# Kernel optimization log

Measured on AMD Instinct MI355X. Metric: run time of the kernel, lower is better.

Reference implementation:

```python
import jax, jax.numpy as jnp
import numpy as np

NH, NKV, HD = 32, 8, 64
ROPE_BASE = 10000.0


def _rope_tables(L, hd):
    inv_freq = 1.0 / (ROPE_BASE ** (jnp.arange(0, hd, 2, dtype=jnp.float32) / hd))
    t = jnp.arange(L, dtype=jnp.float32)
    freqs = jnp.outer(t, inv_freq)              # (L, hd/2)
    emb = jnp.concatenate([freqs, freqs], -1)   # (L, hd)
    return jnp.cos(emb), jnp.sin(emb)


def _rotate_half(x):
    h = x.shape[-1] // 2
    return jnp.concatenate([-x[..., h:], x[..., :h]], axis=-1)


def _apply_rope(x, cos, sin):
    # x: (B, H, L, hd); cos/sin: (L, hd) broadcast over B, H
    return x * cos[None, None] + _rotate_half(x) * sin[None, None]


def setup_inputs() -> dict:
    key = jax.random.key(0)
    ks = jax.random.split(key, 5)
    B, L, H = 2, 2048, 2048
    s = 0.02
    return {
        "x": jax.random.normal(ks[0], (B, L, H), dtype=jnp.float32),
        "wq": jax.random.normal(ks[1], (NH * HD, H), dtype=jnp.float32) * s,
        "wk": jax.random.normal(ks[2], (NKV * HD, H), dtype=jnp.float32) * s,
        "wv": jax.random.normal(ks[3], (NKV * HD, H), dtype=jnp.float32) * s,
        "wo": jax.random.normal(ks[4], (H, NH * HD), dtype=jnp.float32) * s,
    }


def reference(x, wq, wk, wv, wo):
    B, L, H = x.shape
    rep = NH // NKV
    q = (x @ wq.T).reshape(B, L, NH, HD).transpose(0, 2, 1, 3)    # (B, nh, L, hd)
    k = (x @ wk.T).reshape(B, L, NKV, HD).transpose(0, 2, 1, 3)   # (B, nkv, L, hd)
    v = (x @ wv.T).reshape(B, L, NKV, HD).transpose(0, 2, 1, 3)
    cos, sin = _rope_tables(L, HD)
    q = _apply_rope(q, cos, sin)
    k = _apply_rope(k, cos, sin)
    # GQA: group q heads instead of repeating K/V (same math as repeat_interleave)
    qg = q.reshape(B, NKV, rep, L, HD)
    scores = jnp.einsum("bgrqd,bgkd->bgrqk", qg, k) / jnp.sqrt(jnp.float32(HD))
    causal = jnp.tril(jnp.ones((L, L), dtype=bool))
    scores = jnp.where(causal, scores, jnp.float32(-jnp.inf))
    probs = jax.nn.softmax(scores, axis=-1)
    out = jnp.einsum("bgrqk,bgkd->bgrqd", probs, v)               # (B, nkv, rep, L, hd)
    out = out.reshape(B, NH, L, HD).transpose(0, 2, 1, 3).reshape(B, L, NH * HD)
    return out @ wo.T
```

## Files before the change

kernel.cpp:

```cpp
#include <hip/hip_runtime.h>

using u16 = unsigned short;
using u32 = unsigned int;
typedef __attribute__((ext_vector_type(8))) short bf16x8;
typedef __attribute__((ext_vector_type(4))) float f32x4;
typedef __attribute__((ext_vector_type(4))) float float4v;
typedef __attribute__((ext_vector_type(4))) unsigned short us4;
typedef __attribute__((ext_vector_type(2))) unsigned int u32x2;

__device__ __forceinline__ u16 f2bf(float f) {
  union { float f; unsigned u; } v; v.f = f;
  unsigned r = v.u + 0x7fffu + ((v.u >> 16) & 1u);
  return (u16)(r >> 16);
}

__device__ __forceinline__ u32 cvtpk(float a, float b) {
  u32 r;
  asm("v_cvt_pk_bf16_f32 %0, %1, %2" : "=v"(r) : "v"(a), "v"(b));
  return r;
}

__device__ __forceinline__ void glds16(const void* g, void* l) {
  __builtin_amdgcn_global_load_lds(
      (const __attribute__((address_space(1))) void*)g,
      (__attribute__((address_space(3))) void*)l, 16, 0, 0);
}

__device__ __forceinline__ void lgkm0() {
  asm volatile("s_waitcnt lgkmcnt(0)" ::: "memory");
}

#define TILE_GATE()                                      \
  asm volatile("s_waitcnt vmcnt(0)" ::: "memory");       \
  __builtin_amdgcn_s_barrier();                          \
  __builtin_amdgcn_sched_barrier(0);

#define MFMA(a, b, c) __builtin_amdgcn_mfma_f32_16x16x32_bf16((a), (b), (c), 0, 0, 0)

#define QSCALE 0.1803368801111601f

__global__ __launch_bounds__(256) void cvt_all(
    const float* __restrict__ x, const float* __restrict__ wq,
    const float* __restrict__ wk, const float* __restrict__ wv,
    const float* __restrict__ wo, u16* __restrict__ x_bf,
    u16* __restrict__ wqkv, u16* __restrict__ wo_bf) {
  int i = blockIdx.x * 256 + threadIdx.x;
  const float4v* src;
  us4* dst;
  if (i < 2097152) {
    src = (const float4v*)x + i; dst = (us4*)x_bf + i;
  } else if (i < 3145728) {
    int j = i - 2097152; src = (const float4v*)wq + j; dst = (us4*)wqkv + j;
  } else if (i < 3407872) {
    int j = i - 3145728; src = (const float4v*)wk + j; dst = (us4*)wqkv + 1048576 + j;
  } else if (i < 3670016) {
    int j = i - 3407872; src = (const float4v*)wv + j; dst = (us4*)wqkv + 1310720 + j;
  } else {
    int j = i - 3670016; src = (const float4v*)wo + j; dst = (us4*)wo_bf + j;
  }
  float4v v = *src;
  us4 o;
  o[0] = f2bf(v[0]); o[1] = f2bf(v[1]); o[2] = f2bf(v[2]); o[3] = f2bf(v[3]);
  *dst = o;
}

__global__ __launch_bounds__(256) void rope_cs(float2* __restrict__ cs) {
  int i = blockIdx.x * 256 + threadIdx.x;
  if (i >= 2048 * 32) return;
  int t = i >> 5, fi = i & 31;
  float inv = powf(10000.f, -(float)fi / 32.f);
  float ang = (float)t * inv;
  cs[i] = make_float2(cosf(ang), sinf(ang));
}

__global__ __launch_bounds__(512, 2) void gemm_qkv(const u16* __restrict__ Ag,
                                                   const u16* __restrict__ Bg,
                                                   const float2* __restrict__ cs,
                                                   u16* __restrict__ q_r,
                                                   u16* __restrict__ k_r,
                                                   u16* __restrict__ v_t) {
  __shared__ u16 Al[2][256 * 64];
  __shared__ u16 Bl[2][256 * 64];

  const int nwg = gridDim.x;
  const int cpx = nwg >> 3;
  const int flat = blockIdx.x;
  const int swb = (flat & 7) * cpx + (flat >> 3);
  const int bx = swb & 15, by = swb >> 4;
  const int bmRow = bx * 256, bnRow = by * 256;

  const int tid = threadIdx.x;
  const int w = tid >> 6, l = tid & 63;
  const int wm = w >> 2, wn = w & 3;
  const int lr = l & 15, lg = l >> 4;
  const int rb7 = lr & 7;

  const int srow = l >> 3;
  const int sch = (l & 7) ^ srow;
  const int reg0 = w * 32;
  const u16* a_src = Ag + (size_t)(bmRow + reg0 + srow) * 2048 + sch * 8;
  const u16* b_src = Bg + (size_t)(bnRow + reg0 + srow) * 2048 + sch * 8;

  auto stageTile = [&](int kt, int bufi) {
    const int kc = kt * 64;
#pragma unroll
    for (int i = 0; i < 4; ++i)
      glds16(a_src + (size_t)i * 8 * 2048 + kc, &Al[bufi][(reg0 + i * 8) * 64]);
#pragma unroll
    for (int i = 0; i < 4; ++i)
      glds16(b_src + (size_t)i * 8 * 2048 + kc, &Bl[bufi][(reg0 + i * 8) * 64]);
  };
  auto rd = [&](const u16* base, int row, int g) -> bf16x8 {
    return *(const bf16x8*)((const char*)base + row * 128 + (((g) ^ rb7) << 4));
  };

  f32x4 acc[8][4];
#pragma unroll
  for (int m = 0; m < 8; ++m)
#pragma unroll
    for (int n = 0; n < 4; ++n) acc[m][n] = f32x4{0.f, 0.f, 0.f, 0.f};

  bf16x8 af[4][2], bfr[4][2];
  const int NT = 32;

  stageTile(0, 0);
  for (int t = 0; t < NT; ++t) {
    const int cur = t & 1;
    const u16* Ab = &Al[cur][0];
    const u16* Bb = &Bl[cur][0];

    TILE_GATE()
    if (t + 1 < NT) stageTile(t + 1, cur ^ 1);

#pragma unroll
    for (int m = 0; m < 4; ++m)
#pragma unroll
      for (int kk = 0; kk < 2; ++kk)
        af[m][kk] = rd(Ab, wm * 128 + m * 16 + lr, kk * 4 + lg);
#pragma unroll
    for (int n = 0; n < 2; ++n)
#pragma unroll
      for (int kk = 0; kk < 2; ++kk)
        bfr[n][kk] = rd(Bb, wn * 64 + n * 16 + lr, kk * 4 + lg);
    __builtin_amdgcn_s_barrier();
    __builtin_amdgcn_s_setprio(1);
#pragma unroll
    for (int m = 0; m < 4; ++m)
#pragma unroll
      for (int n = 0; n < 2; ++n)
#pragma unroll
        for (int kk = 0; kk < 2; ++kk)
          acc[m][n] = MFMA(af[m][kk], bfr[n][kk], acc[m][n]);
    __builtin_amdgcn_s_setprio(0);
    __builtin_amdgcn_s_barrier();

#pragma unroll
    for (int n = 2; n < 4; ++n)
#pragma unroll
      for (int kk = 0; kk < 2; ++kk)
        bfr[n][kk] = rd(Bb, wn * 64 + n * 16 + lr, kk * 4 + lg);
    __builtin_amdgcn_s_barrier();
    __builtin_amdgcn_s_setprio(1);
#pragma unroll
    for (int m = 0; m < 4; ++m)
#pragma unroll
      for (int n = 2; n < 4; ++n)
#pragma unroll
        for (int kk = 0; kk < 2; ++kk)
          acc[m][n] = MFMA(af[m][kk], bfr[n][kk], acc[m][n]);
    __builtin_amdgcn_s_setprio(0);
    __builtin_amdgcn_s_barrier();

#pragma unroll
    for (int m = 0; m < 4; ++m)
#pragma unroll
      for (int kk = 0; kk < 2; ++kk)
        af[m][kk] = rd(Ab, wm * 128 + 64 + m * 16 + lr, kk * 4 + lg);
    __builtin_amdgcn_s_barrier();
    __builtin_amdgcn_s_setprio(1);
#pragma unroll
    for (int m = 0; m < 4; ++m)
#pragma unroll
      for (int n = 0; n < 2; ++n)
#pragma unroll
        for (int kk = 0; kk < 2; ++kk)
          acc[4 + m][n] = MFMA(af[m][kk], bfr[n][kk], acc[4 + m][n]);
    __builtin_amdgcn_s_setprio(0);
    __builtin_amdgcn_s_barrier();

    __builtin_amdgcn_s_setprio(1);
#pragma unroll
    for (int m = 0; m < 4; ++m)
#pragma unroll
      for (int n = 2; n < 4; ++n)
#pragma unroll
        for (int kk = 0; kk < 2; ++kk)
          acc[4 + m][n] = MFMA(af[m][kk], bfr[n][kk], acc[4 + m][n]);
    __builtin_amdgcn_s_setprio(0);
  }

  const int cbcol = bnRow + wn * 64;
  const int rowbase = bmRow + wm * 128;

  if (cbcol < 2560) {
    const bool isQ = (cbcol < 2048);
    const int h = (isQ ? cbcol : cbcol - 2048) >> 6;
    u16* dst = isQ ? q_r : k_r;
    const int nh = isQ ? 32 : 8;
#pragma unroll
    for (int m = 0; m < 8; ++m) {
#pragma unroll
      for (int j = 0; j < 4; ++j) {
        const int row = rowbase + m * 16 + lg * 4 + j;
        const int b = row >> 11, ll = row & 2047;
        const float2 c0 = cs[ll * 32 + lr];
        const float2 c1 = cs[ll * 32 + 16 + lr];
        u16* op = dst + (((size_t)b * nh + h) * 2048 + ll) * 64;
#pragma unroll
        for (int n = 0; n < 4; ++n) {
          const float val = acc[m][n][j];
          const float oth = acc[m][n ^ 2][j];
          const float cx = (n & 1) ? c1.x : c0.x;
          const float sy = (n & 1) ? c1.y : c0.y;
          float r = (n < 2) ? (val * cx - oth * sy) : (val * cx + oth * sy);
          if (isQ) r *= QSCALE;
          op[n * 16 + lr] = f2bf(r);
        }
      }
    }
  } else {
    const int h = (cbcol - 2560) >> 6;
#pragma unroll
    for (int m = 0; m < 8; ++m) {
      const int row0 = rowbase + m * 16 + lg * 4;
      const int b = row0 >> 11, l0 = row0 & 2047;
#pragma unroll
      for (int n = 0; n < 4; ++n) {
        const int d = n * 16 + lr;
        us4 pk;
#pragma unroll
        for (int j = 0; j < 4; ++j) pk[j] = f2bf(acc[m][n][j]);
        *(us4*)&v_t[(((size_t)b * 8 + h) * 64 + d) * 2048 + l0] = pk;
      }
    }
  }
}

__global__ __launch_bounds__(512, 2) void gemm_o(const u16* __restrict__ Ag,
                                                 const u16* __restrict__ Bg,
                                                 float* __restrict__ C) {
  __shared__ u16 Al[2][256 * 64];
  __shared__ u16 Bl[2][128 * 64];

  const int nwg = gridDim.x;
  const int cpx = nwg >> 3;
  const int flat = blockIdx.x;
  const int swb = (flat & 7) * cpx + (flat >> 3);
  const int bx = swb & 15, by = swb >> 4;
  const int bmRow = bx * 256, bnRow = by * 128;

  const int tid = threadIdx.x;
  const int w = tid >> 6, l = tid & 63;
  const int wm = w >> 1, wn = w & 1;
  const int lr = l & 15, lg = l >> 4;
  const int rb7 = lr & 7;

  const int srow = l >> 3;
  const int sch = (l & 7) ^ srow;
  const int areg = w * 32;
  const int breg = w * 16;
  const u16* a_src = Ag + (size_t)(bmRow + areg + srow) * 2048 + sch * 8;
  const u16* b_src = Bg + (size_t)(bnRow + breg + srow) * 2048 + sch * 8;

  auto stageTile = [&](int kt, int bufi) {
    const int kc = kt * 64;
#pragma unroll
    for (int i = 0; i < 4; ++i)
      glds16(a_src + (size_t)i * 8 * 2048 + kc, &Al[bufi][(areg + i * 8) * 64]);
#pragma unroll
    for (int i = 0; i < 2; ++i)
      glds16(b_src + (size_t)i * 8 * 2048 + kc, &Bl[bufi][(breg + i * 8) * 64]);
  };
  auto rd = [&](const u16* base, int row, int g) -> bf16x8 {
    return *(const bf16x8*)((const char*)base + row * 128 + (((g) ^ rb7) << 4));
  };

  f32x4 acc[4][4];
#pragma unroll
  for (int m = 0; m < 4; ++m)
#pragma unroll
    for (int n = 0; n < 4; ++n) acc[m][n] = f32x4{0.f, 0.f, 0.f, 0.f};

  bf16x8 af[4][2], bfr[4][2];
  const int NT = 32;

  stageTile(0, 0);
  for (int t = 0; t < NT; ++t) {
    const int cur = t & 1;
    const u16* Ab = &Al[cur][0];
    const u16* Bb = &Bl[cur][0];

    TILE_GATE()
    if (t + 1 < NT) stageTile(t + 1, cur ^ 1);

#pragma unroll
    for (int m = 0; m < 4; ++m)
#pragma unroll
      for (int kk = 0; kk < 2; ++kk)
        af[m][kk] = rd(Ab, wm * 64 + m * 16 + lr, kk * 4 + lg);
#pragma unroll
    for (int n = 0; n < 2; ++n)
#pragma unroll
      for (int kk = 0; kk < 2; ++kk)
        bfr[n][kk] = rd(Bb, wn * 64 + n * 16 + lr, kk * 4 + lg);
    __builtin_amdgcn_s_barrier();
    __builtin_amdgcn_s_setprio(1);
#pragma unroll
    for (int m = 0; m < 4; ++m)
#pragma unroll
      for (int n = 0; n < 2; ++n)
#pragma unroll
        for (int kk = 0; kk < 2; ++kk)
          acc[m][n] = MFMA(af[m][kk], bfr[n][kk], acc[m][n]);
    __builtin_amdgcn_s_setprio(0);
    __builtin_amdgcn_s_barrier();

#pragma unroll
    for (int n = 2; n < 4; ++n)
#pragma unroll
      for (int kk = 0; kk < 2; ++kk)
        bfr[n][kk] = rd(Bb, wn * 64 + n * 16 + lr, kk * 4 + lg);
    __builtin_amdgcn_s_barrier();
    __builtin_amdgcn_s_setprio(1);
#pragma unroll
    for (int m = 0; m < 4; ++m)
#pragma unroll
      for (int n = 2; n < 4; ++n)
#pragma unroll
        for (int kk = 0; kk < 2; ++kk)
          acc[m][n] = MFMA(af[m][kk], bfr[n][kk], acc[m][n]);
    __builtin_amdgcn_s_setprio(0);
  }

  float* Cp = C + (size_t)(bmRow + wm * 64) * 2048 + bnRow + wn * 64;
#pragma unroll
  for (int m = 0; m < 4; ++m)
#pragma unroll
    for (int n = 0; n < 4; ++n)
#pragma unroll
      for (int j = 0; j < 4; ++j)
        Cp[(size_t)(m * 16 + lg * 4 + j) * 2048 + n * 16 + lr] = acc[m][n][j];
}

__global__ __launch_bounds__(256) void attn4(const u16* __restrict__ q_r,
                                             const u16* __restrict__ k_r,
                                             const u16* __restrict__ v_t,
                                             u16* __restrict__ attn_o) {
  __shared__ u16 Kl[2][64 * 64];
  __shared__ u16 Vl[2][64 * 64];
  __shared__ u16 Pl[4][32 * 64];

  const int bid = blockIdx.x;
  const int q0 = (63 - (bid >> 4)) * 32;
  const int bk = bid & 15;
  const int b = bk >> 3, kvh = bk & 7;

  const int tid = threadIdx.x;
  const int w = tid >> 6;
  const int l = tid & 63;
  const int h = kvh * 4 + w;
  const int lr = l & 15, lg = l >> 4;

  const u16* Qp = q_r + (((size_t)(b * 32 + h)) * 2048 + q0) * 64;
  const u16* Kp = k_r + ((size_t)(b * 8 + kvh)) * 2048 * 64;
  const u16* Vp = v_t + ((size_t)(b * 8 + kvh)) * 64 * 2048;

  bf16x8 qf[2][2];
#pragma unroll
  for (int qh = 0; qh < 2; ++qh)
#pragma unroll
    for (int kh = 0; kh < 2; ++kh)
      qf[qh][kh] = *(const bf16x8*)&Qp[(qh * 16 + lr) * 64 + kh * 32 + lg * 8];

  bf16x8 ones;
#pragma unroll
  for (int i = 0; i < 8; ++i) ones[i] = (short)0x3F80;

  f32x4 o[2][4];
#pragma unroll
  for (int qh = 0; qh < 2; ++qh)
#pragma unroll
    for (int nf = 0; nf < 4; ++nf) o[qh][nf] = f32x4{0.f, 0.f, 0.f, 0.f};
  f32x4 lsv[2] = {f32x4{0.f, 0.f, 0.f, 0.f}, f32x4{0.f, 0.f, 0.f, 0.f}};

  const int sr = l >> 3;
  const int sc = (l & 7) ^ sr;
  const int nt = (q0 + 95) >> 6;
  const int nfull = q0 >> 6;

  auto stage = [&](int bufi, int t) {
#pragma unroll
    for (int p = 0; p < 2; ++p) {
      const int r = p * 32 + w * 8 + sr;
      glds16(Kp + (size_t)(t * 64 + r) * 64 + sc * 8, &Kl[bufi][(p * 32 + w * 8) * 64]);
      glds16(Vp + (size_t)r * 2048 + t * 64 + sc * 8, &Vl[bufi][(p * 32 + w * 8) * 64]);
    }
  };

  stage(0, 0);
  int buf = 0;
  for (int t = 0; t < nt; ++t) {
    __syncthreads();
    if (t + 1 < nt) stage(buf ^ 1, t + 1);
    const int kv0 = t * 64;

    f32x4 s[2][4];
#pragma unroll
    for (int qh = 0; qh < 2; ++qh)
#pragma unroll
      for (int kv4 = 0; kv4 < 4; ++kv4) s[qh][kv4] = f32x4{0.f, 0.f, 0.f, 0.f};
    const int swz = (lr & 7) << 4;
#pragma unroll
    for (int kv4 = 0; kv4 < 4; ++kv4) {
      const int kvr = kv4 * 16 + lr;
#pragma unroll
      for (int kh = 0; kh < 2; ++kh) {
        bf16x8 kf = *(const bf16x8*)((const char*)&Kl[buf][kvr * 64] +
                                     ((kh * 64 + lg * 16) ^ swz));
        s[0][kv4] = MFMA(kf, qf[0][kh], s[0][kv4]);
        s[1][kv4] = MFMA(kf, qf[1][kh], s[1][kv4]);
      }
    }

    const bool diag = (t >= nfull);
#pragma unroll
    for (int qh = 0; qh < 2; ++qh) {
      const int qrow = q0 + qh * 16 + lr;
      if (diag) {
#pragma unroll
        for (int kv4 = 0; kv4 < 4; ++kv4)
#pragma unroll
          for (int j = 0; j < 4; ++j)
            if ((kv0 + kv4 * 16 + lg * 4 + j) > qrow) s[qh][kv4][j] = -1e30f;
      }
#pragma unroll
      for (int kv4 = 0; kv4 < 4; ++kv4) {
        u32x2 pk;
        pk[0] = cvtpk(exp2f(s[qh][kv4][0]), exp2f(s[qh][kv4][1]));
        pk[1] = cvtpk(exp2f(s[qh][kv4][2]), exp2f(s[qh][kv4][3]));
        *(u32x2*)((char*)&Pl[w][(qh * 16 + lr) * 64] +
                  ((kv4 * 32 + lg * 8) ^ swz)) = pk;
      }
    }

    lgkm0();
#pragma unroll
    for (int k2 = 0; k2 < 2; ++k2) {
      bf16x8 pa[2];
#pragma unroll
      for (int qh = 0; qh < 2; ++qh)
        pa[qh] = *(const bf16x8*)((const char*)&Pl[w][(qh * 16 + lr) * 64] +
                                  ((k2 * 64 + lg * 16) ^ swz));
      lsv[0] = MFMA(pa[0], ones, lsv[0]);
      lsv[1] = MFMA(pa[1], ones, lsv[1]);
#pragma unroll
      for (int nf = 0; nf < 4; ++nf) {
        const int d = nf * 16 + lr;
        bf16x8 bv = *(const bf16x8*)((const char*)&Vl[buf][d * 64] +
                                     ((k2 * 64 + lg * 16) ^ swz));
        o[0][nf] = MFMA(pa[0], bv, o[0][nf]);
        o[1][nf] = MFMA(pa[1], bv, o[1][nf]);
      }
    }
    buf ^= 1;
  }

  u16* Op = attn_o + (size_t)b * 2048 * 2048 + h * 64;
#pragma unroll
  for (int qh = 0; qh < 2; ++qh) {
#pragma unroll
    for (int j = 0; j < 4; ++j) {
      const float inv = __builtin_amdgcn_rcpf(lsv[qh][j]);
      const int row = q0 + qh * 16 + lg * 4 + j;
#pragma unroll
      for (int nf = 0; nf < 4; ++nf)
        Op[(size_t)row * 2048 + nf * 16 + lr] = f2bf(o[qh][nf][j] * inv);
    }
  }
}

extern "C" void kernel_launch(void* const* d_in, const int* in_sizes, int n_in,
                              void* d_out, int out_size, void* d_ws, size_t ws_size,
                              hipStream_t stream) {
  const float* x = (const float*)d_in[0];
  const float* wq = (const float*)d_in[1];
  const float* wk = (const float*)d_in[2];
  const float* wv = (const float*)d_in[3];
  const float* wo = (const float*)d_in[4];
  float* out = (float*)d_out;

  char* p = (char*)d_ws;
  auto alloc = [&](size_t bytes) {
    char* r = p;
    p += (bytes + 255) & ~(size_t)255;
    return r;
  };
  u16* x_bf    = (u16*)alloc((size_t)8388608 * 2);
  u16* wqkv    = (u16*)alloc((size_t)3072 * 2048 * 2);
  u16* wo_bf   = (u16*)alloc((size_t)2048 * 2048 * 2);
  u16* q_r     = (u16*)alloc((size_t)8388608 * 2);
  u16* k_r     = (u16*)alloc((size_t)2097152 * 2);
  u16* v_t     = (u16*)alloc((size_t)2097152 * 2);
  u16* attn_o  = (u16*)alloc((size_t)8388608 * 2);
  float2* cs   = (float2*)alloc((size_t)65536 * 8);

  cvt_all<<<18432, 256, 0, stream>>>(x, wq, wk, wv, wo, x_bf, wqkv, wo_bf);
  rope_cs<<<256, 256, 0, stream>>>(cs);

  gemm_qkv<<<192, 512, 0, stream>>>(x_bf, wqkv, cs, q_r, k_r, v_t);

  attn4<<<1024, 256, 0, stream>>>(q_r, k_r, v_t, attn_o);

  gemm_o<<<256, 512, 0, stream>>>(attn_o, wo_bf, out);
}
```

Measured before the change: 318.2 us.

## Overlap next-tile global loads with compute via partial vmcnt waits, drop inner barriers

In both the QKV-projection and output-projection GEMM loops, the next tile's global-to-LDS loads are now issued before waiting. The wait then uses a partial vmcnt count, so only the current tile's loads must finish while the next tile's stay in flight. The intra-iteration barriers that split the MFMA work into four phases are removed: all B fragments are loaded at once and MFMAs run in two larger groups. This cuts barrier overhead and exposed memory latency, at the cost of more live registers and a dependence on the hardcoded vmcnt values matching the number of loads per stage.

```diff
diff --git a/kernel.cpp b/kernel.cpp
--- a/kernel.cpp
+++ b/kernel.cpp
@@ -30,10 +30,7 @@
   asm volatile("s_waitcnt lgkmcnt(0)" ::: "memory");
 }
 
-#define TILE_GATE()                                      \
-  asm volatile("s_waitcnt vmcnt(0)" ::: "memory");       \
-  __builtin_amdgcn_s_barrier();                          \
-  __builtin_amdgcn_sched_barrier(0);
+#define SCHED0() __builtin_amdgcn_sched_barrier(0)
 
 #define MFMA(a, b, c) __builtin_amdgcn_mfma_f32_16x16x32_bf16((a), (b), (c), 0, 0, 0)
 
@@ -129,8 +126,16 @@
     const u16* Ab = &Al[cur][0];
     const u16* Bb = &Bl[cur][0];
 
-    TILE_GATE()
-    if (t + 1 < NT) stageTile(t + 1, cur ^ 1);
+    __builtin_amdgcn_s_barrier();
+    SCHED0();
+    if (t + 1 < NT) {
+      stageTile(t + 1, cur ^ 1);
+      asm volatile("s_waitcnt vmcnt(8)" ::: "memory");
+    } else {
+      asm volatile("s_waitcnt vmcnt(0)" ::: "memory");
+    }
+    __builtin_amdgcn_s_barrier();
+    SCHED0();
 
 #pragma unroll
     for (int m = 0; m < 4; ++m)
@@ -138,61 +143,29 @@
       for (int kk = 0; kk < 2; ++kk)
         af[m][kk] = rd(Ab, wm * 128 + m * 16 + lr, kk * 4 + lg);
 #pragma unroll
-    for (int n = 0; n < 2; ++n)
+    for (int n = 0; n < 4; ++n)
 #pragma unroll
       for (int kk = 0; kk < 2; ++kk)
         bfr[n][kk] = rd(Bb, wn * 64 + n * 16 + lr, kk * 4 + lg);
-    __builtin_amdgcn_s_barrier();
     __builtin_amdgcn_s_setprio(1);
 #pragma unroll
     for (int m = 0; m < 4; ++m)
 #pragma unroll
-      for (int n = 0; n < 2; ++n)
+      for (int n = 0; n < 4; ++n)
 #pragma unroll
         for (int kk = 0; kk < 2; ++kk)
           acc[m][n] = MFMA(af[m][kk], bfr[n][kk], acc[m][n]);
     __builtin_amdgcn_s_setprio(0);
-    __builtin_amdgcn_s_barrier();
-
-#pragma unroll
-    for (int n = 2; n < 4; ++n)
-#pragma unroll
-      for (int kk = 0; kk < 2; ++kk)
-        bfr[n][kk] = rd(Bb, wn * 64 + n * 16 + lr, kk * 4 + lg);
-    __builtin_amdgcn_s_barrier();
-    __builtin_amdgcn_s_setprio(1);
-#pragma unroll
-    for (int m = 0; m < 4; ++m)
-#pragma unroll
-      for (int n = 2; n < 4; ++n)
-#pragma unroll
-        for (int kk = 0; kk < 2; ++kk)
-          acc[m][n] = MFMA(af[m][kk], bfr[n][kk], acc[m][n]);
-    __builtin_amdgcn_s_setprio(0);
-    __builtin_amdgcn_s_barrier();
-
 #pragma unroll
     for (int m = 0; m < 4; ++m)
 #pragma unroll
       for (int kk = 0; kk < 2; ++kk)
         af[m][kk] = rd(Ab, wm * 128 + 64 + m * 16 + lr, kk * 4 + lg);
-    __builtin_amdgcn_s_barrier();
     __builtin_amdgcn_s_setprio(1);
 #pragma unroll
     for (int m = 0; m < 4; ++m)
 #pragma unroll
-      for (int n = 0; n < 2; ++n)
-#pragma unroll
-        for (int kk = 0; kk < 2; ++kk)
-          acc[4 + m][n] = MFMA(af[m][kk], bfr[n][kk], acc[4 + m][n]);
-    __builtin_amdgcn_s_setprio(0);
-    __builtin_amdgcn_s_barrier();
-
-    __builtin_amdgcn_s_setprio(1);
-#pragma unroll
-    for (int m = 0; m < 4; ++m)
-#pragma unroll
-      for (int n = 2; n < 4; ++n)
+      for (int n = 0; n < 4; ++n)
 #pragma unroll
         for (int kk = 0; kk < 2; ++kk)
           acc[4 + m][n] = MFMA(af[m][kk], bfr[n][kk], acc[4 + m][n]);
@@ -300,8 +273,16 @@
     const u16* Ab = &Al[cur][0];
     const u16* Bb = &Bl[cur][0];
 
-    TILE_GATE()
-    if (t + 1 < NT) stageTile(t + 1, cur ^ 1);
+    __builtin_amdgcn_s_barrier();
+    SCHED0();
+    if (t + 1 < NT) {
+      stageTile(t + 1, cur ^ 1);
+      asm volatile("s_waitcnt vmcnt(6)" ::: "memory");
+    } else {
+      asm volatile("s_waitcnt vmcnt(0)" ::: "memory");
+    }
+    __builtin_amdgcn_s_barrier();
+    SCHED0();
 
 #pragma unroll
     for (int m = 0; m < 4; ++m)
@@ -309,33 +290,15 @@
       for (int kk = 0; kk < 2; ++kk)
         af[m][kk] = rd(Ab, wm * 64 + m * 16 + lr, kk * 4 + lg);
 #pragma unroll
-    for (int n = 0; n < 2; ++n)
+    for (int n = 0; n < 4; ++n)
 #pragma unroll
       for (int kk = 0; kk < 2; ++kk)
         bfr[n][kk] = rd(Bb, wn * 64 + n * 16 + lr, kk * 4 + lg);
-    __builtin_amdgcn_s_barrier();
     __builtin_amdgcn_s_setprio(1);
 #pragma unroll
     for (int m = 0; m < 4; ++m)
 #pragma unroll
-      for (int n = 0; n < 2; ++n)
-#pragma unroll
-        for (int kk = 0; kk < 2; ++kk)
-          acc[m][n] = MFMA(af[m][kk], bfr[n][kk], acc[m][n]);
-    __builtin_amdgcn_s_setprio(0);
-    __builtin_amdgcn_s_barrier();
-
-#pragma unroll
-    for (int n = 2; n < 4; ++n)
-#pragma unroll
-      for (int kk = 0; kk < 2; ++kk)
-        bfr[n][kk] = rd(Bb, wn * 64 + n * 16 + lr, kk * 4 + lg);
-    __builtin_amdgcn_s_barrier();
-    __builtin_amdgcn_s_setprio(1);
-#pragma unroll
-    for (int m = 0; m < 4; ++m)
-#pragma unroll
-      for (int n = 2; n < 4; ++n)
+      for (int n = 0; n < 4; ++n)
 #pragma unroll
         for (int kk = 0; kk < 2; ++kk)
           acc[m][n] = MFMA(af[m][kk], bfr[n][kk], acc[m][n]);
```

After: 301.8 us. 5.2% less time.
